# Performance work log

Hardware: AMD Instinct MI355X
Metric: run time of the kernel (lower is better)

## Reference

```python
import jax, jax.numpy as jnp
import numpy as np
from jax import lax

H = 64  # hidden size


def _lstm_layer(x, w_ih, w_hh, b_ih, b_hh):
    """Single LSTM layer, batch_first x: [B, T, D] -> [B, T, H].
    PyTorch gate order: i, f, g, o."""
    B = x.shape[0]
    # Precompute input projections for all timesteps: [T, B, 4H]
    xg = jnp.einsum('btd,gd->tbg', x, w_ih) + (b_ih + b_hh)

    def step(carry, xg_t):
        h, c = carry
        gates = xg_t + h @ w_hh.T  # [B, 4H]
        i, f, g, o = jnp.split(gates, 4, axis=-1)
        i = jax.nn.sigmoid(i)
        f = jax.nn.sigmoid(f)
        g = jnp.tanh(g)
        o = jax.nn.sigmoid(o)
        c = f * c + i * g
        h = o * jnp.tanh(c)
        return (h, c), h

    h0 = jnp.zeros((B, H), dtype=x.dtype)
    c0 = jnp.zeros((B, H), dtype=x.dtype)
    (_, _), hs = lax.scan(step, (h0, c0), xg)  # hs: [T, B, H]
    return jnp.swapaxes(hs, 0, 1)  # [B, T, H]


def setup_inputs() -> dict:
    key = jax.random.key(0)
    ks = jax.random.split(key, 11)
    s = 1.0 / np.sqrt(H)  # PyTorch LSTM init scale
    x = jax.random.normal(ks[0], (8192, 168, 7), dtype=jnp.float32)
    return {
        'x': x,
        'w_ih0': jax.random.normal(ks[1], (4 * H, 7), jnp.float32) * s,
        'w_hh0': jax.random.normal(ks[2], (4 * H, H), jnp.float32) * s,
        'b_ih0': jax.random.normal(ks[3], (4 * H,), jnp.float32) * s,
        'b_hh0': jax.random.normal(ks[4], (4 * H,), jnp.float32) * s,
        'w_ih1': jax.random.normal(ks[5], (4 * H, H), jnp.float32) * s,
        'w_hh1': jax.random.normal(ks[6], (4 * H, H), jnp.float32) * s,
        'b_ih1': jax.random.normal(ks[7], (4 * H,), jnp.float32) * s,
        'b_hh1': jax.random.normal(ks[8], (4 * H,), jnp.float32) * s,
        'fc_w': jax.random.normal(ks[9], (4, H), jnp.float32) * s,
        'fc_b': jax.random.normal(ks[10], (4,), jnp.float32) * s,
    }


def reference(x, w_ih0, w_hh0, b_ih0, b_hh0, w_ih1, w_hh1, b_ih1, b_hh1, fc_w, fc_b):
    h1 = _lstm_layer(x, w_ih0, w_hh0, b_ih0, b_hh0)   # [B, T, H]
    h2 = _lstm_layer(h1, w_ih1, w_hh1, b_ih1, b_hh1)  # [B, T, H]
    last = h2[:, -1, :]                               # dropout is identity in eval
    return last @ fc_w.T + fc_b                       # [B, 4]
```

## Files before the change

### kernel.cpp

```cpp
#include <hip/hip_runtime.h>

#define TT 168
#define HH 64
#define DD 7
#define NS 16
#define BB 8192
#define CH 8
#define NTH 512

typedef float f32x4 __attribute__((ext_vector_type(4)));
typedef _Float16 f16x8 __attribute__((ext_vector_type(8)));

#define MFMA16F(A, B, C) __builtin_amdgcn_mfma_f32_16x16x32_f16((A), (B), (C), 0, 0, 0)

__device__ __forceinline__ f16x8 pack8(f32x4 a, f32x4 b) {
    f16x8 r;
#pragma unroll
    for (int e = 0; e < 4; ++e) { r[e] = (_Float16)a[e]; r[4 + e] = (_Float16)b[e]; }
    return r;
}

__device__ __forceinline__ float sigf(float v) {
    return __builtin_amdgcn_rcpf(1.0f + __builtin_amdgcn_exp2f(v * -1.44269504f));
}
__device__ __forceinline__ float thf(float v) {
    return fmaf(-2.0f, __builtin_amdgcn_rcpf(__builtin_amdgcn_exp2f(v * 2.88539008f) + 1.0f), 1.0f);
}

__device__ __forceinline__ void cell_update(const f32x4& gi, const f32x4& gf,
                                            const f32x4& gg, const f32x4& go,
                                            f32x4& cst, _Float16* dst) {
    f32x4 hv;
#pragma unroll
    for (int r = 0; r < 4; ++r) {
        const float iv = sigf(gi[r]), fv = sigf(gf[r]);
        const float gv = thf(gg[r]),  ov = sigf(go[r]);
        cst[r] = fv * cst[r] + iv * gv;
        hv[r] = ov * thf(cst[r]);
    }
    unsigned d0, d1;
    asm("v_cvt_pkrtz_f16_f32 %0, %1, %2" : "=v"(d0) : "v"(hv[0]), "v"(hv[1]));
    asm("v_cvt_pkrtz_f16_f32 %0, %1, %2" : "=v"(d1) : "v"(hv[2]), "v"(hv[3]));
    *(uint2*)dst = make_uint2(d0, d1);
}

__global__ __launch_bounds__(NTH, 4)
void weather_lstm_mfma(const float* __restrict__ x,
                       const float* __restrict__ w_ih0, const float* __restrict__ w_hh0,
                       const float* __restrict__ b_ih0, const float* __restrict__ b_hh0,
                       const float* __restrict__ w_ih1, const float* __restrict__ w_hh1,
                       const float* __restrict__ b_ih1, const float* __restrict__ b_hh1,
                       const float* __restrict__ fc_w, const float* __restrict__ fc_b,
                       float* __restrict__ out)
{
    __shared__ f16x8 xs[2][CH][NS];
    __shared__ __align__(16) _Float16 h1[2][NS][72];
    __shared__ __align__(16) _Float16 h2[2][NS][72];

    const int tid  = threadIdx.x;
    const int wv   = tid >> 6;
    const int q    = wv & 3;
    const int lane = tid & 63;
    const int col  = lane & 15;
    const int kg   = lane >> 4;
    const int s0   = blockIdx.x * NS;
    const int ub   = 16 * q + 4 * kg;

    for (int i = tid; i < 2 * NS * 72; i += NTH) {
        ((short*)h1)[i] = 0; ((short*)h2)[i] = 0;
    }
    if (tid < CH * NS) {
        const int tloc = tid >> 4, ss = tid & 15;
        const float* px = x + ((size_t)(s0 + ss) * TT + tloc) * DD;
        f32x4 a, b;
        a[0] = px[0]; a[1] = px[1]; a[2] = px[2]; a[3] = px[3];
        b[0] = px[4]; b[1] = px[5]; b[2] = px[6]; b[3] = 1.0f;
        xs[0][tloc][ss] = pack8(a, b);
    }
    __syncthreads();

    const f16x8 z8 = {0, 0, 0, 0, 0, 0, 0, 0};
    const f32x4 zz = {0, 0, 0, 0};

    if (wv < 4) {
        f16x8 W0[4][2], WX[4];
#pragma unroll
        for (int t4 = 0; t4 < 4; ++t4) {
            const int row = 64 * t4 + 16 * q + col;
#pragma unroll
            for (int kf = 0; kf < 2; ++kf) {
                const float* p = w_hh0 + (size_t)row * HH + 32 * kf + 8 * kg;
                W0[t4][kf] = pack8(*(const f32x4*)p, *(const f32x4*)(p + 4));
            }
            f32x4 a = {0, 0, 0, 0}, b = {0, 0, 0, 0};
            if (kg == 0) {
                const float* p = w_ih0 + (size_t)row * DD;
                a[0] = p[0]; a[1] = p[1]; a[2] = p[2]; a[3] = p[3];
                b[0] = p[4]; b[1] = p[5]; b[2] = p[6];
                b[3] = b_ih0[row] + b_hh0[row];
            }
            WX[t4] = pack8(a, b);
        }
        f32x4 c1 = {0, 0, 0, 0};

#pragma unroll 1
        for (int k = 0; k <= TT + 1; ++k) {
            f32x4 aA[4];
            if (k < TT) {
                if (tid < CH * NS && (k & 7) == 0 && k + CH < TT) {
                    const int tloc = tid >> 4, ss = tid & 15;
                    const int tg = k + CH + tloc;
                    const float* px = x + ((size_t)(s0 + ss) * TT + tg) * DD;
                    f32x4 a, b;
                    a[0] = px[0]; a[1] = px[1]; a[2] = px[2]; a[3] = px[3];
                    b[0] = px[4]; b[1] = px[5]; b[2] = px[6]; b[3] = 1.0f;
                    const int nb = ((k >> 3) & 1) ^ 1;
                    xs[nb][tloc][ss] = pack8(a, b);
                }
                const int cb = (k >> 3) & 1, tt = k & 7;
                const int rp = (k - 1) & 1;

                __builtin_amdgcn_s_setprio(1);
                f16x8 ax = z8;
                if (kg == 0) ax = xs[cb][tt][col];
                aA[0] = MFMA16F(WX[0], ax, zz);
                aA[1] = MFMA16F(WX[1], ax, zz);
                aA[2] = MFMA16F(WX[2], ax, zz);
                aA[3] = MFMA16F(WX[3], ax, zz);
#pragma unroll
                for (int kf = 0; kf < 2; ++kf) {
                    const f16x8 dh = *(const f16x8*)&h1[rp][col][32 * kf + 8 * kg];
                    aA[0] = MFMA16F(W0[0][kf], dh, aA[0]);
                    aA[1] = MFMA16F(W0[1][kf], dh, aA[1]);
                    aA[2] = MFMA16F(W0[2][kf], dh, aA[2]);
                    aA[3] = MFMA16F(W0[3][kf], dh, aA[3]);
                }
                __builtin_amdgcn_s_setprio(0);
            }
            __syncthreads();
            if (k < TT) {
                const int wp = k & 1;
                cell_update(aA[0], aA[1], aA[2], aA[3], c1, &h1[wp][col][ub]);
            }
            __syncthreads();
        }
    } else {
        f16x8 W1[4][4];
        f32x4 bias1[4];
#pragma unroll
        for (int t4 = 0; t4 < 4; ++t4) {
            const int row = 64 * t4 + 16 * q + col;
            const int rr  = 64 * t4 + 16 * q + 4 * kg;
            bias1[t4] = *(const f32x4*)(b_ih1 + rr) + *(const f32x4*)(b_hh1 + rr);
#pragma unroll
            for (int kf = 0; kf < 4; ++kf) {
                const float* base = (kf < 2) ? (w_ih1 + (size_t)row * HH + 32 * kf)
                                             : (w_hh1 + (size_t)row * HH + 32 * (kf - 2));
                const float* p = base + 8 * kg;
                W1[t4][kf] = pack8(*(const f32x4*)p, *(const f32x4*)(p + 4));
            }
        }
        f32x4 c2 = {0, 0, 0, 0};
        f32x4 aB[4];

#pragma unroll 1
        for (int k = 0; k <= TT + 1; ++k) {
            if (k >= 2) {
                const int wp = k & 1;
                cell_update(aB[0], aB[1], aB[2], aB[3], c2, &h2[wp][col][ub]);
            }
            __syncthreads();
            if (k >= 1 && k <= TT) {
                const int rp1 = (k - 1) & 1;
                const int rp2 = k & 1;
                __builtin_amdgcn_s_setprio(1);
                {
                    const f16x8 dh = *(const f16x8*)&h1[rp1][col][8 * kg];
                    aB[0] = MFMA16F(W1[0][0], dh, bias1[0]);
                    aB[1] = MFMA16F(W1[1][0], dh, bias1[1]);
                    aB[2] = MFMA16F(W1[2][0], dh, bias1[2]);
                    aB[3] = MFMA16F(W1[3][0], dh, bias1[3]);
                }
                {
                    const f16x8 dh = *(const f16x8*)&h1[rp1][col][32 + 8 * kg];
                    aB[0] = MFMA16F(W1[0][1], dh, aB[0]);
                    aB[1] = MFMA16F(W1[1][1], dh, aB[1]);
                    aB[2] = MFMA16F(W1[2][1], dh, aB[2]);
                    aB[3] = MFMA16F(W1[3][1], dh, aB[3]);
                }
#pragma unroll
                for (int kf = 0; kf < 2; ++kf) {
                    const f16x8 eh = *(const f16x8*)&h2[rp2][col][32 * kf + 8 * kg];
                    aB[0] = MFMA16F(W1[0][kf + 2], eh, aB[0]);
                    aB[1] = MFMA16F(W1[1][kf + 2], eh, aB[1]);
                    aB[2] = MFMA16F(W1[2][kf + 2], eh, aB[2]);
                    aB[3] = MFMA16F(W1[3][kf + 2], eh, aB[3]);
                }
                __builtin_amdgcn_s_setprio(0);
            }
            __syncthreads();
        }
    }

    if (tid < NS * 4) {
        const int s = tid >> 2, k = tid & 3;
        float a = fc_b[k];
#pragma unroll
        for (int j = 0; j < HH; ++j)
            a = fmaf((float)h2[1][s][j], fc_w[k * HH + j], a);
        out[(size_t)(s0 + s) * 4 + k] = a;
    }
}

extern "C" void kernel_launch(void* const* d_in, const int* in_sizes, int n_in,
                              void* d_out, int out_size, void* d_ws, size_t ws_size,
                              hipStream_t stream) {
    const float* x     = (const float*)d_in[0];
    const float* w_ih0 = (const float*)d_in[1];
    const float* w_hh0 = (const float*)d_in[2];
    const float* b_ih0 = (const float*)d_in[3];
    const float* b_hh0 = (const float*)d_in[4];
    const float* w_ih1 = (const float*)d_in[5];
    const float* w_hh1 = (const float*)d_in[6];
    const float* b_ih1 = (const float*)d_in[7];
    const float* b_hh1 = (const float*)d_in[8];
    const float* fc_w  = (const float*)d_in[9];
    const float* fc_b  = (const float*)d_in[10];
    float* out = (float*)d_out;

    dim3 grid(BB / NS), block(NTH);
    weather_lstm_mfma<<<grid, block, 0, stream>>>(
        x, w_ih0, w_hh0, b_ih0, b_hh0,
        w_ih1, w_hh1, b_ih1, b_hh1, fc_w, fc_b, out);
}
```

Before: 249.9 us.

## Fold activation scales into weights and halve per-step barriers in LSTM loop

```diff
diff --git a/kernel.cpp b/kernel.cpp
--- a/kernel.cpp
+++ b/kernel.cpp
@@ -20,23 +20,23 @@
     return r;
 }
 
-__device__ __forceinline__ float sigf(float v) {
-    return __builtin_amdgcn_rcpf(1.0f + __builtin_amdgcn_exp2f(v * -1.44269504f));
-}
-__device__ __forceinline__ float thf(float v) {
-    return fmaf(-2.0f, __builtin_amdgcn_rcpf(__builtin_amdgcn_exp2f(v * 2.88539008f) + 1.0f), 1.0f);
-}
-
-__device__ __forceinline__ void cell_update(const f32x4& gi, const f32x4& gf,
-                                            const f32x4& gg, const f32x4& go,
+__device__ __forceinline__ void cell_update(const f32x4& si, const f32x4& sf,
+                                            const f32x4& sg, const f32x4& so,
                                             f32x4& cst, _Float16* dst) {
     f32x4 hv;
 #pragma unroll
     for (int r = 0; r < 4; ++r) {
-        const float iv = sigf(gi[r]), fv = sigf(gf[r]);
-        const float gv = thf(gg[r]),  ov = sigf(go[r]);
-        cst[r] = fv * cst[r] + iv * gv;
-        hv[r] = ov * thf(cst[r]);
+        const float uf = __builtin_amdgcn_exp2f(sf[r]);
+        const float fv = __builtin_amdgcn_rcpf(1.0f + uf);
+        const float ui = __builtin_amdgcn_exp2f(si[r]);
+        const float ug = __builtin_amdgcn_exp2f(fminf(sg[r], 80.0f));
+        const float R1 = __builtin_amdgcn_rcpf((1.0f + ui) * (1.0f + ug));
+        const float ig = (1.0f - ug) * R1;
+        cst[r] = fv * cst[r] + ig;
+        const float uo = __builtin_amdgcn_exp2f(so[r]);
+        const float uc = __builtin_amdgcn_exp2f(fminf(cst[r] * -2.88539008f, 80.0f));
+        const float R2 = __builtin_amdgcn_rcpf((1.0f + uo) * (1.0f + uc));
+        hv[r] = (1.0f - uc) * R2;
     }
     unsigned d0, d1;
     asm("v_cvt_pkrtz_f16_f32 %0, %1, %2" : "=v"(d0) : "v"(hv[0]), "v"(hv[1]));
@@ -86,11 +86,12 @@
         f16x8 W0[4][2], WX[4];
 #pragma unroll
         for (int t4 = 0; t4 < 4; ++t4) {
+            const float sc = (t4 == 2) ? -2.88539008f : -1.44269504f;
             const int row = 64 * t4 + 16 * q + col;
 #pragma unroll
             for (int kf = 0; kf < 2; ++kf) {
                 const float* p = w_hh0 + (size_t)row * HH + 32 * kf + 8 * kg;
-                W0[t4][kf] = pack8(*(const f32x4*)p, *(const f32x4*)(p + 4));
+                W0[t4][kf] = pack8(*(const f32x4*)p * sc, *(const f32x4*)(p + 4) * sc);
             }
             f32x4 a = {0, 0, 0, 0}, b = {0, 0, 0, 0};
             if (kg == 0) {
@@ -99,13 +100,12 @@
                 b[0] = p[4]; b[1] = p[5]; b[2] = p[6];
                 b[3] = b_ih0[row] + b_hh0[row];
             }
-            WX[t4] = pack8(a, b);
+            WX[t4] = pack8(a * sc, b * sc);
         }
         f32x4 c1 = {0, 0, 0, 0};
 
 #pragma unroll 1
-        for (int k = 0; k <= TT + 1; ++k) {
-            f32x4 aA[4];
+        for (int k = 0; k <= TT; ++k) {
             if (k < TT) {
                 if (tid < CH * NS && (k & 7) == 0 && k + CH < TT) {
                     const int tloc = tid >> 4, ss = tid & 15;
@@ -120,6 +120,7 @@
                 const int cb = (k >> 3) & 1, tt = k & 7;
                 const int rp = (k - 1) & 1;
 
+                f32x4 aA[4];
                 __builtin_amdgcn_s_setprio(1);
                 f16x8 ax = z8;
                 if (kg == 0) ax = xs[cb][tt][col];
@@ -136,11 +137,7 @@
                     aA[3] = MFMA16F(W0[3][kf], dh, aA[3]);
                 }
                 __builtin_amdgcn_s_setprio(0);
-            }
-            __syncthreads();
-            if (k < TT) {
-                const int wp = k & 1;
-                cell_update(aA[0], aA[1], aA[2], aA[3], c1, &h1[wp][col][ub]);
+                cell_update(aA[0], aA[1], aA[2], aA[3], c1, &h1[k & 1][col][ub]);
             }
             __syncthreads();
         }
@@ -149,30 +146,26 @@
         f32x4 bias1[4];
 #pragma unroll
         for (int t4 = 0; t4 < 4; ++t4) {
+            const float sc = (t4 == 2) ? -2.88539008f : -1.44269504f;
             const int row = 64 * t4 + 16 * q + col;
             const int rr  = 64 * t4 + 16 * q + 4 * kg;
-            bias1[t4] = *(const f32x4*)(b_ih1 + rr) + *(const f32x4*)(b_hh1 + rr);
+            bias1[t4] = (*(const f32x4*)(b_ih1 + rr) + *(const f32x4*)(b_hh1 + rr)) * sc;
 #pragma unroll
             for (int kf = 0; kf < 4; ++kf) {
                 const float* base = (kf < 2) ? (w_ih1 + (size_t)row * HH + 32 * kf)
                                              : (w_hh1 + (size_t)row * HH + 32 * (kf - 2));
                 const float* p = base + 8 * kg;
-                W1[t4][kf] = pack8(*(const f32x4*)p, *(const f32x4*)(p + 4));
+                W1[t4][kf] = pack8(*(const f32x4*)p * sc, *(const f32x4*)(p + 4) * sc);
             }
         }
         f32x4 c2 = {0, 0, 0, 0};
-        f32x4 aB[4];
 
 #pragma unroll 1
-        for (int k = 0; k <= TT + 1; ++k) {
-            if (k >= 2) {
-                const int wp = k & 1;
-                cell_update(aB[0], aB[1], aB[2], aB[3], c2, &h2[wp][col][ub]);
-            }
-            __syncthreads();
-            if (k >= 1 && k <= TT) {
+        for (int k = 0; k <= TT; ++k) {
+            if (k >= 1) {
                 const int rp1 = (k - 1) & 1;
                 const int rp2 = k & 1;
+                f32x4 aB[4];
                 __builtin_amdgcn_s_setprio(1);
                 {
                     const f16x8 dh = *(const f16x8*)&h1[rp1][col][8 * kg];
@@ -197,6 +190,7 @@
                     aB[3] = MFMA16F(W1[3][kf + 2], eh, aB[3]);
                 }
                 __builtin_amdgcn_s_setprio(0);
+                cell_update(aB[0], aB[1], aB[2], aB[3], c2, &h2[(k - 1) & 1][col][ub]);
             }
             __syncthreads();
         }
```

Result: faster. 238.6 us (-4.6%).
